# Optimization experiments

Measured on AMD Instinct MI355X. Metric: run time of the kernel, lower is better.

## Reference

```python
import jax, jax.numpy as jnp
import numpy as np

D = 1024   # rnn_size
H = 64     # pooling MLP hidden
B, C = 16, 1024


def setup_inputs() -> dict:
    key = jax.random.key(0)
    ks = jax.random.split(key, 12)
    s = 1.0 / np.sqrt(D)
    inp = {
        "encoder_outputs": jax.random.normal(ks[0], (B, C, D), jnp.float32),
        # Linear weights stored as [in, out] (y = x @ W + b), same math as torch Linear
        "Wf": jax.random.uniform(ks[1], (D, D), jnp.float32, -s, s),
        "bf": jax.random.uniform(ks[2], (D,), jnp.float32, -s, s),
        "Wg": jax.random.uniform(ks[3], (D, D), jnp.float32, -s, s),
        "bg": jax.random.uniform(ks[4], (D,), jnp.float32, -s, s),
        "Wx": jax.random.uniform(ks[5], (D, D), jnp.float32, -s, s),
        "bx": jax.random.uniform(ks[6], (D,), jnp.float32, -s, s),
        "W1": jax.random.uniform(ks[7], (D, H), jnp.float32, -s, s),
        "b1": jax.random.uniform(ks[8], (H,), jnp.float32, -s, s),
        "W2": jax.random.uniform(ks[9], (H, 1), jnp.float32, -1.0 / np.sqrt(H), 1.0 / np.sqrt(H)),
        "b2": jax.random.uniform(ks[10], (1,), jnp.float32, -1.0 / np.sqrt(H), 1.0 / np.sqrt(H)),
        # gamma is nn.Parameter(zeros(1)); use a nonzero value for a nontrivial baseline
        "gamma": jax.random.normal(ks[11], (1,), jnp.float32) * 0.1,
    }
    return inp


def reference(encoder_outputs, Wf, bf, Wg, bg, Wx, bx, W1, b1, W2, b2, gamma):
    x = encoder_outputs                                  # [B, C, D]
    q = jax.nn.relu(x @ Wf + bf)                         # proj_query [B, C, D]
    k = jax.nn.relu(x @ Wg + bg)                         # proj_key   [B, C, D]
    v = jax.nn.relu(x @ Wx + bx)                         # proj_value [B, C, D]
    energy = jnp.einsum('bid,bjd->bij', q, k)            # [B, C, C]
    attn = jax.nn.softmax(energy, axis=1)                # softmax over dim=1 (non-standard axis)
    # out = attention^T @ v : out[b,j,d] = sum_i attn[b,i,j] * v[b,i,d]
    out = jnp.einsum('bij,bid->bjd', attn, v)            # [B, C, D]
    out = gamma * out + x                                # gamma-residual
    # MLP attention pooling over C
    e2 = jax.nn.relu(x @ W1 + b1) @ W2 + b2              # [B, C, 1]
    w = jax.nn.softmax(e2[..., 0], axis=1)               # [B, C]
    return jnp.sum(out * w[..., None], axis=1)           # [B, D]
```

## Files before the change

### kernel.cpp

```cpp
#include <hip/hip_runtime.h>

#define B_ 16
#define C_ 1024
#define D_ 1024
#define H_ 64
#define M_ (B_*C_)

typedef __attribute__((ext_vector_type(8))) short bf16x8;
typedef __attribute__((ext_vector_type(8))) unsigned short ushortx8;
typedef __attribute__((ext_vector_type(4))) float f32x4;

__device__ __forceinline__ float wave_max(float v){
  #pragma unroll
  for (int o = 32; o > 0; o >>= 1) v = fmaxf(v, __shfl_xor(v, o));
  return v;
}
__device__ __forceinline__ float wave_sum(float v){
  #pragma unroll
  for (int o = 32; o > 0; o >>= 1) v += __shfl_xor(v, o);
  return v;
}

__device__ __forceinline__ ushort f2bf(float f){
  union { float f; unsigned u; } a; a.f = f;
  unsigned r = a.u + 0x7fff + ((a.u >> 16) & 1);
  return (ushort)(r >> 16);
}
__device__ __forceinline__ float bf2f(ushort h){
  union { unsigned u; float f; } a; a.u = ((unsigned)h) << 16; return a.f;
}

__device__ __forceinline__ void lds_cp16(const ushort* g, ushort* l){
  __builtin_amdgcn_global_load_lds(
      (const __attribute__((address_space(1))) void*)g,
      (__attribute__((address_space(3))) void*)l, 16, 0, 0);
}

__global__ __launch_bounds__(256) void prep_kernel(
    const float* __restrict__ x, const float* __restrict__ Wf,
    const float* __restrict__ Wg, const float* __restrict__ Wx,
    const float* __restrict__ W1,
    ushort* __restrict__ x_bf, ushort* __restrict__ wt,
    ushort* __restrict__ w1t)
{
  __shared__ float tile[32][33];
  const int blk = blockIdx.x;
  const int t = threadIdx.x;
  if (blk < 16384) {
    const int i = blk*256 + t;
    float4 v = ((const float4*)x)[i];
    ushort4 o;
    o.x = f2bf(v.x); o.y = f2bf(v.y); o.z = f2bf(v.z); o.w = f2bf(v.w);
    ((ushort4*)x_bf)[i] = o;
  } else if (blk < 16384 + 3072) {
    const int bb = blk - 16384;
    const int z = bb >> 10, rem = bb & 1023;
    const int n0 = (rem & 31)*32, k0 = (rem >> 5)*32;
    const float* W = (z == 0) ? Wf : (z == 1) ? Wg : Wx;
    ushort* Out = wt + (size_t)z*D_*D_;
    const int tx = t & 31, ty = t >> 5;
    #pragma unroll
    for (int i = 0; i < 32; i += 8)
      tile[ty+i][tx] = W[(size_t)(k0+ty+i)*D_ + n0+tx];
    __syncthreads();
    #pragma unroll
    for (int i = 0; i < 32; i += 8)
      Out[(size_t)(n0+ty+i)*D_ + k0+tx] = f2bf(tile[tx][ty+i]);
  } else {
    const int bb = blk - 16384 - 3072;
    const int n0 = (bb & 1)*32, k0 = (bb >> 1)*32;
    const int tx = t & 31, ty = t >> 5;
    #pragma unroll
    for (int i = 0; i < 32; i += 8)
      tile[ty+i][tx] = W1[(size_t)(k0+ty+i)*H_ + n0+tx];
    __syncthreads();
    #pragma unroll
    for (int i = 0; i < 32; i += 8)
      w1t[(size_t)(n0+ty+i)*D_ + k0+tx] = f2bf(tile[tx][ty+i]);
  }
}

__global__ __launch_bounds__(256, 3) void proj_kernel(
    const ushort* __restrict__ A, const ushort* __restrict__ Wt,
    const float* __restrict__ bf, const float* __restrict__ bg,
    const float* __restrict__ bx,
    ushort* __restrict__ q, ushort* __restrict__ k, ushort* __restrict__ v)
{
  __shared__ ushort As[128*64];
  __shared__ ushort Bs[128*64];
  const int t = threadIdx.x;
  const int wid = t >> 6, lane = t & 63;
  const int m0 = blockIdx.y * 128, n0 = blockIdx.x * 128;
  const int seg = n0 >> 10;
  const int nloc0 = n0 - (seg << 10);

  const int srow = t >> 3;
  const int sch = ((t & 7) ^ (srow & 7)) * 8;
  const ushort* gaBase = A  + (size_t)(m0 + srow)*1024 + sch;
  const ushort* gbBase = Wt + (size_t)(n0 + srow)*1024 + sch;

  const int quad = lane >> 4, l16 = lane & 15;
  const int wm = wid >> 1, wn = wid & 1;
  const int cx0 = ((0*4 + quad) ^ (l16 & 7)) * 8;
  const int cx1 = ((1*4 + quad) ^ (l16 & 7)) * 8;
  const int arow0 = (wm*64 + l16)*64;
  const int brow0 = (wn*64 + l16)*64;

  f32x4 acc[4][4] = {};

  for (int k0 = 0; k0 < 1024; k0 += 64) {
    #pragma unroll
    for (int i = 0; i < 4; ++i) {
      lds_cp16(gaBase + (size_t)(i*32)*1024, As + (8*wid + 32*i)*64);
      lds_cp16(gbBase + (size_t)(i*32)*1024, Bs + (8*wid + 32*i)*64);
    }
    gaBase += 64; gbBase += 64;
    __syncthreads();
    #pragma unroll
    for (int h = 0; h < 2; ++h) {
      const int cx = h ? cx1 : cx0;
      bf16x8 af[4], bfr[4];
      #pragma unroll
      for (int i = 0; i < 4; ++i) {
        af[i]  = *(const bf16x8*)&As[arow0 + i*1024 + cx];
        bfr[i] = *(const bf16x8*)&Bs[brow0 + i*1024 + cx];
      }
      #pragma unroll
      for (int mt = 0; mt < 4; ++mt)
        #pragma unroll
        for (int nt = 0; nt < 4; ++nt)
          acc[mt][nt] = __builtin_amdgcn_mfma_f32_16x16x32_bf16(
              af[mt], bfr[nt], acc[mt][nt], 0, 0, 0);
    }
    __syncthreads();
  }

  const float* bp = (seg == 0) ? bf : (seg == 1) ? bg : bx;
  ushort* op      = (seg == 0) ? q  : (seg == 1) ? k  : v;
  const int gm_base = m0 + wm*64 + quad*4;
  const int gn_base = nloc0 + wn*64 + l16;
  float bv[4];
  #pragma unroll
  for (int nt = 0; nt < 4; ++nt) bv[nt] = bp[gn_base + nt*16];
  #pragma unroll
  for (int mt = 0; mt < 4; ++mt)
    #pragma unroll
    for (int rr = 0; rr < 4; ++rr) {
      const size_t rowoff = (size_t)(gm_base + mt*16 + rr) * 1024;
      #pragma unroll
      for (int nt = 0; nt < 4; ++nt)
        op[rowoff + gn_base + nt*16] =
            f2bf(fmaxf(acc[mt][nt][rr] + bv[nt], 0.f));
    }
}

__global__ __launch_bounds__(256, 4) void energy_kernel(
    const ushort* __restrict__ Km, const ushort* __restrict__ Qm,
    ushort* __restrict__ E)
{
  __shared__ ushort As[64*64];
  __shared__ ushort Bs[128*64];
  const int t = threadIdx.x;
  const int wid = t >> 6, lane = t & 63;
  const int m0 = blockIdx.y * 64, n0 = blockIdx.x * 128;
  const int bz = blockIdx.z;
  const ushort* Ab = Km + (size_t)bz * C_ * D_;
  const ushort* Bb = Qm + (size_t)bz * C_ * D_;

  const int srow = t >> 3;
  const int sch = ((t & 7) ^ (srow & 7)) * 8;
  const ushort* gaBase = Ab + (size_t)(m0 + srow)*1024 + sch;
  const ushort* gbBase = Bb + (size_t)(n0 + srow)*1024 + sch;

  const int quad = lane >> 4, l16 = lane & 15;
  const int cx0 = ((0*4 + quad) ^ (l16 & 7)) * 8;
  const int cx1 = ((1*4 + quad) ^ (l16 & 7)) * 8;
  const int brow0 = (wid*32 + l16)*64;

  f32x4 acc[4][2] = {};

  for (int k0 = 0; k0 < 1024; k0 += 64) {
    #pragma unroll
    for (int i = 0; i < 2; ++i)
      lds_cp16(gaBase + (size_t)(i*32)*1024, As + (8*wid + 32*i)*64);
    #pragma unroll
    for (int i = 0; i < 4; ++i)
      lds_cp16(gbBase + (size_t)(i*32)*1024, Bs + (8*wid + 32*i)*64);
    gaBase += 64; gbBase += 64;
    __syncthreads();
    #pragma unroll
    for (int h = 0; h < 2; ++h) {
      const int cx = h ? cx1 : cx0;
      bf16x8 af[4], bfr[2];
      #pragma unroll
      for (int i = 0; i < 4; ++i)
        af[i] = *(const bf16x8*)&As[(i*16 + l16)*64 + cx];
      #pragma unroll
      for (int i = 0; i < 2; ++i)
        bfr[i] = *(const bf16x8*)&Bs[brow0 + i*16*64 + cx];
      #pragma unroll
      for (int mt = 0; mt < 4; ++mt)
        #pragma unroll
        for (int nt = 0; nt < 2; ++nt)
          acc[mt][nt] = __builtin_amdgcn_mfma_f32_16x16x32_bf16(
              af[mt], bfr[nt], acc[mt][nt], 0, 0, 0);
    }
    __syncthreads();
  }

  ushort* O = E + (size_t)bz * C_ * C_;
  const int gm_base = m0 + quad*4;
  const int gn_base = n0 + wid*32 + l16;
  #pragma unroll
  for (int mt = 0; mt < 4; ++mt)
    #pragma unroll
    for (int rr = 0; rr < 4; ++rr) {
      const size_t rowoff = (size_t)(gm_base + mt*16 + rr) * 1024;
      #pragma unroll
      for (int nt = 0; nt < 2; ++nt)
        O[rowoff + gn_base + nt*16] = f2bf(acc[mt][nt][rr]);
    }
}

__device__ __forceinline__ int fsw(int row){
  return (row & 3) ^ ((row >> 2) & 3);
}
__global__ __launch_bounds__(256) void pool_mfma_kernel(
    const ushort* __restrict__ A, const ushort* __restrict__ Bt,
    const float* __restrict__ b1, const float* __restrict__ W2,
    float* __restrict__ e2out)
{
  __shared__ ushort As[128*32];
  __shared__ ushort Bs[64*32];
  const int t = threadIdx.x;
  const int wid = t >> 6, lane = t & 63;
  const int m0 = blockIdx.x * 128;

  const int r = t >> 2;
  const int kc = ((t & 3) ^ fsw(r)) * 8;
  const ushort* ga0 = A + (size_t)(m0 + r)*1024 + kc;
  const ushort* ga1 = ga0 + (size_t)64*1024;
  const ushort* gb0 = Bt + (size_t)r*1024 + kc;
  ushort* lA = As + wid*512;
  ushort* lB = Bs + wid*512;

  const int quad = lane >> 4, l16 = lane & 15;
  const int fr = fsw(l16);
  const int am0 = (wid*32 + l16)*32 + ((quad ^ fr)*8);
  const int bn0 = l16*32 + ((quad ^ fr)*8);

  f32x4 acc[2][4] = {};

  for (int k0 = 0; k0 < 1024; k0 += 32) {
    lds_cp16(ga0, lA); lds_cp16(ga1, lA + 2048);
    lds_cp16(gb0, lB);
    ga0 += 32; ga1 += 32; gb0 += 32;
    __syncthreads();
    bf16x8 af[2], bfr[4];
    #pragma unroll
    for (int i = 0; i < 2; ++i) af[i] = *(const bf16x8*)&As[am0 + i*512];
    #pragma unroll
    for (int i = 0; i < 4; ++i) bfr[i] = *(const bf16x8*)&Bs[bn0 + i*512];
    #pragma unroll
    for (int mt = 0; mt < 2; ++mt)
      #pragma unroll
      for (int nt = 0; nt < 4; ++nt)
        acc[mt][nt] = __builtin_amdgcn_mfma_f32_16x16x32_bf16(
            af[mt], bfr[nt], acc[mt][nt], 0, 0, 0);
    __syncthreads();
  }

  float b1v[4], w2v[4];
  #pragma unroll
  for (int nt = 0; nt < 4; ++nt) {
    b1v[nt] = b1[nt*16 + l16];
    w2v[nt] = W2[nt*16 + l16];
  }
  #pragma unroll
  for (int mt = 0; mt < 2; ++mt)
    #pragma unroll
    for (int rr = 0; rr < 4; ++rr) {
      float h = 0.f;
      #pragma unroll
      for (int nt = 0; nt < 4; ++nt)
        h += fmaxf(acc[mt][nt][rr] + b1v[nt], 0.f) * w2v[nt];
      #pragma unroll
      for (int o = 1; o < 16; o <<= 1) h += __shfl_xor(h, o);
      if (l16 == 0)
        e2out[m0 + wid*32 + mt*16 + quad*4 + rr] = h;
    }
}

__global__ __launch_bounds__(256) void fused_sm_kernel(
    const ushort* __restrict__ E, const float* __restrict__ w,
    float* __restrict__ u_part)
{
  __shared__ float ul[4][1024];
  const int b = blockIdx.y;
  const int strip = blockIdx.x;
  const int t = threadIdx.x, wv = t >> 6, lane = t & 63;
  const ushort* Eb = E + (size_t)b*C_*C_;
  const float* wb = w + (size_t)b*C_;
  float acc[2][8] = {};
  #pragma unroll
  for (int rj = 0; rj < 4; ++rj) {
    const int j = strip*16 + wv*4 + rj;
    const ushort* row = Eb + (size_t)j*C_;
    float vv[2][8];
    float m = -1e30f;
    #pragma unroll
    for (int c = 0; c < 2; ++c) {
      ushortx8 h = *(const ushortx8*)&row[c*512 + lane*8];
      #pragma unroll
      for (int kk = 0; kk < 8; ++kk) {
        vv[c][kk] = bf2f(h[kk]);
        m = fmaxf(m, vv[c][kk]);
      }
    }
    m = wave_max(m);
    float e[2][8];
    float s = 0.f;
    #pragma unroll
    for (int c = 0; c < 2; ++c)
      #pragma unroll
      for (int kk = 0; kk < 8; ++kk) {
        e[c][kk] = expf(vv[c][kk] - m);
        s += e[c][kk];
      }
    s = wave_sum(s);
    const float sc = wb[j] / s;
    #pragma unroll
    for (int c = 0; c < 2; ++c)
      #pragma unroll
      for (int kk = 0; kk < 8; ++kk) acc[c][kk] += sc * e[c][kk];
  }
  #pragma unroll
  for (int c = 0; c < 2; ++c)
    #pragma unroll
    for (int k4 = 0; k4 < 2; ++k4) {
      float4 o;
      o.x = acc[c][k4*4+0]; o.y = acc[c][k4*4+1];
      o.z = acc[c][k4*4+2]; o.w = acc[c][k4*4+3];
      *(float4*)&ul[wv][c*512 + lane*8 + k4*4] = o;
    }
  __syncthreads();
  float4 r0 = *(float4*)&ul[0][t*4];
  float4 r1 = *(float4*)&ul[1][t*4];
  float4 r2 = *(float4*)&ul[2][t*4];
  float4 r3 = *(float4*)&ul[3][t*4];
  float4 o;
  o.x = r0.x+r1.x+r2.x+r3.x; o.y = r0.y+r1.y+r2.y+r3.y;
  o.z = r0.z+r1.z+r2.z+r3.z; o.w = r0.w+r1.w+r2.w+r3.w;
  *(float4*)&u_part[((size_t)strip*B_ + b)*C_ + t*4] = o;
}

__global__ __launch_bounds__(256) void softmax_w_kernel(
    const float* __restrict__ e2in, float* __restrict__ w)
{
  __shared__ float redm[4];
  __shared__ float reds[4];
  const int b = blockIdx.x, t = threadIdx.x;
  const int lane = t & 63, wid = t >> 6;
  const float* row = e2in + (size_t)b*C_;
  float4 v = *(const float4*)&row[t*4];
  float m = fmaxf(fmaxf(v.x, v.y), fmaxf(v.z, v.w));
  m = wave_max(m);
  if (lane == 0) redm[wid] = m;
  __syncthreads();
  m = fmaxf(fmaxf(redm[0], redm[1]), fmaxf(redm[2], redm[3]));
  float e0 = expf(v.x - m), e1 = expf(v.y - m);
  float e2 = expf(v.z - m), e3 = expf(v.w - m);
  float s = e0 + e1 + e2 + e3;
  s = wave_sum(s);
  if (lane == 0) reds[wid] = s;
  __syncthreads();
  s = reds[0] + reds[1] + reds[2] + reds[3];
  const float inv = 1.0f / s;
  float4 o; o.x = e0*inv; o.y = e1*inv; o.z = e2*inv; o.w = e3*inv;
  *(float4*)&w[(size_t)b*C_ + t*4] = o;
}

__global__ __launch_bounds__(256) void final_part_kernel(
    const ushort* __restrict__ X, const ushort* __restrict__ V,
    const float* __restrict__ u_part, const float* __restrict__ w,
    const float* __restrict__ gamma, float* __restrict__ fpart)
{
  const int b = blockIdx.x, s = blockIdx.y;
  const int t = threadIdx.x;
  __shared__ float red[16][17];
  __shared__ float us[16];
  {
    const int ii = t & 15, g = t >> 4;
    float p = 0.f;
    #pragma unroll
    for (int q2 = 0; q2 < 4; ++q2) {
      const int sp = g*4 + q2;
      p += u_part[((size_t)sp*B_ + b)*C_ + s*16 + ii];
    }
    red[ii][g] = p;
  }
  __syncthreads();
  if (t < 16) {
    float s2 = 0.f;
    #pragma unroll
    for (int g = 0; g < 16; ++g) s2 += red[t][g];
    us[t] = s2;
  }
  __syncthreads();

  const int d0 = t * 4;
  const ushort* xb = X + (size_t)b*C_*D_;
  const ushort* vb = V + (size_t)b*C_*D_;
  const float* wb = w + (size_t)b*C_;
  float4 av = {0,0,0,0}, ax = {0,0,0,0};
  #pragma unroll
  for (int ii = 0; ii < 16; ++ii) {
    const int i = s*16 + ii;
    const float ui = us[ii], wi = wb[i];
    ushort4 vv = *(const ushort4*)&vb[(size_t)i*D_ + d0];
    ushort4 xv = *(const ushort4*)&xb[(size_t)i*D_ + d0];
    av.x += ui*bf2f(vv.x); av.y += ui*bf2f(vv.y);
    av.z += ui*bf2f(vv.z); av.w += ui*bf2f(vv.w);
    ax.x += wi*bf2f(xv.x); ax.y += wi*bf2f(xv.y);
    ax.z += wi*bf2f(xv.z); ax.w += wi*bf2f(xv.w);
  }
  const float g = gamma[0];
  float4 o;
  o.x = g*av.x + ax.x; o.y = g*av.y + ax.y;
  o.z = g*av.z + ax.z; o.w = g*av.w + ax.w;
  *(float4*)&fpart[((size_t)s*B_ + b)*D_ + d0] = o;
}

__global__ __launch_bounds__(256) void final_combine_kernel(
    const float* __restrict__ fpart, float* __restrict__ out)
{
  const int idx = blockIdx.x*256 + threadIdx.x;
  float s = 0.f;
  #pragma unroll 8
  for (int sp = 0; sp < 64; ++sp) s += fpart[(size_t)sp*B_*D_ + idx];
  out[idx] = s;
}

extern "C" void kernel_launch(void* const* d_in, const int* in_sizes, int n_in,
                              void* d_out, int out_size, void* d_ws, size_t ws_size,
                              hipStream_t stream) {
  (void)in_sizes; (void)n_in; (void)out_size; (void)ws_size;
  const float* x  = (const float*)d_in[0];
  const float* Wf = (const float*)d_in[1];
  const float* bf = (const float*)d_in[2];
  const float* Wg = (const float*)d_in[3];
  const float* bg = (const float*)d_in[4];
  const float* Wx = (const float*)d_in[5];
  const float* bx = (const float*)d_in[6];
  const float* W1 = (const float*)d_in[7];
  const float* b1 = (const float*)d_in[8];
  const float* W2 = (const float*)d_in[9];
  const float* gamma = (const float*)d_in[11];
  float* out = (float*)d_out;

  ushort* x_bf = (ushort*)d_ws;
  ushort* wt   = x_bf + (size_t)M_*D_;
  ushort* w1t  = wt + (size_t)3*D_*D_;
  ushort* q_bf = w1t + (size_t)H_*D_;
  ushort* k_bf = q_bf + (size_t)M_*D_;
  ushort* v_bf = k_bf + (size_t)M_*D_;
  ushort* E    = v_bf + (size_t)M_*D_;
  float*  e2b  = (float*)(E + (size_t)B_*C_*C_);
  float*  wbuf = e2b + M_;
  float*  u_part = wbuf + M_;
  float*  fpart  = (float*)E;

  prep_kernel<<<dim3(16384+3072+64), 256, 0, stream>>>(
      x, Wf, Wg, Wx, W1, x_bf, wt, w1t);

  proj_kernel<<<dim3(24,128), 256, 0, stream>>>(x_bf, wt, bf, bg, bx,
                                                q_bf, k_bf, v_bf);

  pool_mfma_kernel<<<dim3(M_/128), 256, 0, stream>>>(x_bf, w1t, b1, W2, e2b);
  softmax_w_kernel<<<dim3(B_), 256, 0, stream>>>(e2b, wbuf);

  energy_kernel<<<dim3(8,16,B_), 256, 0, stream>>>(k_bf, q_bf, E);
  fused_sm_kernel<<<dim3(64,B_), 256, 0, stream>>>(E, wbuf, u_part);

  final_part_kernel<<<dim3(B_,64), 256, 0, stream>>>(x_bf, v_bf, u_part, wbuf,
                                                     gamma, fpart);
  final_combine_kernel<<<dim3(M_/256), 256, 0, stream>>>(fpart, out);
}
```

Measured before the change: 329.9 us.

## Rewrite projection GEMM with 256x256 tiles, 4-stage LDS pipeline and XCD swizzle

```diff
diff --git a/kernel.cpp b/kernel.cpp
--- a/kernel.cpp
+++ b/kernel.cpp
@@ -80,70 +80,113 @@
   }
 }
 
-__global__ __launch_bounds__(256, 3) void proj_kernel(
+__global__ __launch_bounds__(512, 2) void proj_kernel(
     const ushort* __restrict__ A, const ushort* __restrict__ Wt,
     const float* __restrict__ bf, const float* __restrict__ bg,
     const float* __restrict__ bx,
     ushort* __restrict__ q, ushort* __restrict__ k, ushort* __restrict__ v)
 {
-  __shared__ ushort As[128*64];
-  __shared__ ushort Bs[128*64];
+  __shared__ ushort As[4][8192];
+  __shared__ ushort Bs[4][8192];
   const int t = threadIdx.x;
-  const int wid = t >> 6, lane = t & 63;
-  const int m0 = blockIdx.y * 128, n0 = blockIdx.x * 128;
+  const int lane = t & 63;
+  const int wid  = t >> 6;
+  const int wm = wid >> 2;
+  const int wn = wid & 3;
+
+  const int wg = blockIdx.x;
+  const int sw = (wg & 7) * 96 + (wg >> 3);
+  const int mI = sw / 12, nI = sw - mI*12;
+  const int m0 = mI * 256, n0 = nI * 256;
   const int seg = n0 >> 10;
-  const int nloc0 = n0 - (seg << 10);
-
-  const int srow = t >> 3;
-  const int sch = ((t & 7) ^ (srow & 7)) * 8;
-  const ushort* gaBase = A  + (size_t)(m0 + srow)*1024 + sch;
-  const ushort* gbBase = Wt + (size_t)(n0 + srow)*1024 + sch;
+  const int nloc0 = n0 & 1023;
+
+  const int srow = t >> 2;
+  const int sfr  = (srow >> 1) & 3;
+  const int schunk = ((t & 3) ^ sfr) * 8;
+  const ushort* gA0 = A  + (size_t)(m0 + srow)*1024 + schunk;
+  const ushort* gA1 = gA0 + (size_t)128*1024;
+  const ushort* gB0 = Wt + (size_t)(n0 + srow)*1024 + schunk;
+  const ushort* gB1 = gB0 + (size_t)128*1024;
+  const int ldst = t * 8;
 
   const int quad = lane >> 4, l16 = lane & 15;
-  const int wm = wid >> 1, wn = wid & 1;
-  const int cx0 = ((0*4 + quad) ^ (l16 & 7)) * 8;
-  const int cx1 = ((1*4 + quad) ^ (l16 & 7)) * 8;
-  const int arow0 = (wm*64 + l16)*64;
-  const int brow0 = (wn*64 + l16)*64;
-
-  f32x4 acc[4][4] = {};
-
-  for (int k0 = 0; k0 < 1024; k0 += 64) {
-    #pragma unroll
-    for (int i = 0; i < 4; ++i) {
-      lds_cp16(gaBase + (size_t)(i*32)*1024, As + (8*wid + 32*i)*64);
-      lds_cp16(gbBase + (size_t)(i*32)*1024, Bs + (8*wid + 32*i)*64);
-    }
-    gaBase += 64; gbBase += 64;
-    __syncthreads();
-    #pragma unroll
-    for (int h = 0; h < 2; ++h) {
-      const int cx = h ? cx1 : cx0;
-      bf16x8 af[4], bfr[4];
-      #pragma unroll
-      for (int i = 0; i < 4; ++i) {
-        af[i]  = *(const bf16x8*)&As[arow0 + i*1024 + cx];
-        bfr[i] = *(const bf16x8*)&Bs[brow0 + i*1024 + cx];
-      }
-      #pragma unroll
-      for (int mt = 0; mt < 4; ++mt)
-        #pragma unroll
-        for (int nt = 0; nt < 4; ++nt)
-          acc[mt][nt] = __builtin_amdgcn_mfma_f32_16x16x32_bf16(
-              af[mt], bfr[nt], acc[mt][nt], 0, 0, 0);
-    }
-    __syncthreads();
+  const int fr4 = (l16 >> 1) & 3;
+  const int aoff = (wm*128 + l16)*32 + ((quad ^ fr4) * 8);
+  const int boff = (wn*64  + l16)*32 + ((quad ^ fr4) * 8);
+
+  f32x4 acc[8][4] = {};
+
+  #pragma unroll
+  for (int tt = 0; tt < 3; ++tt) {
+    const int ko = tt * 32;
+    lds_cp16(gA0 + ko, &As[tt][ldst]);
+    lds_cp16(gA1 + ko, &As[tt][4096 + ldst]);
+    lds_cp16(gB0 + ko, &Bs[tt][ldst]);
+    lds_cp16(gB1 + ko, &Bs[tt][4096 + ldst]);
+  }
+  asm volatile("s_waitcnt vmcnt(8)" ::: "memory");
+  __builtin_amdgcn_s_barrier();
+
+  for (int t0 = 0; t0 < 32; ++t0) {
+    const int cur = t0 & 3;
+    const ushort* Ab = As[cur];
+    const ushort* Bb = Bs[cur];
+    const int nxt = (t0 + 3) & 3;
+    const int ko  = (t0 + 3) * 32;
+
+    bf16x8 bfr[4], af[4];
+    #pragma unroll
+    for (int i = 0; i < 4; ++i) bfr[i] = *(const bf16x8*)&Bb[boff + i*512];
+    #pragma unroll
+    for (int i = 0; i < 4; ++i) af[i]  = *(const bf16x8*)&Ab[aoff + i*512];
+    if (t0 < 29) {
+      lds_cp16(gA0 + ko, &As[nxt][ldst]);
+      lds_cp16(gA1 + ko, &As[nxt][4096 + ldst]);
+    }
+    __builtin_amdgcn_s_barrier();
+    asm volatile("s_waitcnt lgkmcnt(0)" ::: "memory");
+    __builtin_amdgcn_s_setprio(1);
+    #pragma unroll
+    for (int mt = 0; mt < 4; ++mt)
+      #pragma unroll
+      for (int nt = 0; nt < 4; ++nt)
+        acc[mt][nt] = __builtin_amdgcn_mfma_f32_16x16x32_bf16(
+            af[mt], bfr[nt], acc[mt][nt], 0, 0, 0);
+    __builtin_amdgcn_s_setprio(0);
+    __builtin_amdgcn_s_barrier();
+
+    #pragma unroll
+    for (int i = 0; i < 4; ++i) af[i] = *(const bf16x8*)&Ab[aoff + 2048 + i*512];
+    if (t0 < 29) {
+      lds_cp16(gB0 + ko, &Bs[nxt][ldst]);
+      lds_cp16(gB1 + ko, &Bs[nxt][4096 + ldst]);
+    }
+    __builtin_amdgcn_s_barrier();
+    asm volatile("s_waitcnt lgkmcnt(0)" ::: "memory");
+    __builtin_amdgcn_s_setprio(1);
+    #pragma unroll
+    for (int mt = 0; mt < 4; ++mt)
+      #pragma unroll
+      for (int nt = 0; nt < 4; ++nt)
+        acc[4+mt][nt] = __builtin_amdgcn_mfma_f32_16x16x32_bf16(
+            af[mt], bfr[nt], acc[4+mt][nt], 0, 0, 0);
+    __builtin_amdgcn_s_setprio(0);
+    if (t0 < 29)       asm volatile("s_waitcnt vmcnt(8)" ::: "memory");
+    else if (t0 == 29) asm volatile("s_waitcnt vmcnt(4)" ::: "memory");
+    else if (t0 == 30) asm volatile("s_waitcnt vmcnt(0)" ::: "memory");
+    __builtin_amdgcn_s_barrier();
   }
 
   const float* bp = (seg == 0) ? bf : (seg == 1) ? bg : bx;
   ushort* op      = (seg == 0) ? q  : (seg == 1) ? k  : v;
-  const int gm_base = m0 + wm*64 + quad*4;
+  const int gm_base = m0 + wm*128 + quad*4;
   const int gn_base = nloc0 + wn*64 + l16;
   float bv[4];
   #pragma unroll
   for (int nt = 0; nt < 4; ++nt) bv[nt] = bp[gn_base + nt*16];
   #pragma unroll
-  for (int mt = 0; mt < 4; ++mt)
+  for (int mt = 0; mt < 8; ++mt)
     #pragma unroll
     for (int rr = 0; rr < 4; ++rr) {
       const size_t rowoff = (size_t)(gm_base + mt*16 + rr) * 1024;
@@ -473,8 +516,8 @@
   prep_kernel<<<dim3(16384+3072+64), 256, 0, stream>>>(
       x, Wf, Wg, Wx, W1, x_bf, wt, w1t);
 
-  proj_kernel<<<dim3(24,128), 256, 0, stream>>>(x_bf, wt, bf, bg, bx,
-                                                q_bf, k_bf, v_bf);
+  proj_kernel<<<dim3(768), 512, 0, stream>>>(x_bf, wt, bf, bg, bx,
+                                             q_bf, k_bf, v_bf);
 
   pool_mfma_kernel<<<dim3(M_/128), 256, 0, stream>>>(x_bf, w1t, b1, W2, e2b);
   softmax_w_kernel<<<dim3(B_), 256, 0, stream>>>(e2b, wbuf);
```

Result: no change. 331.9 us (+0.6%).

## Rewrite projection GEMM as 256x256 double-buffered pipelined tile kernel

Applied to the files above, without the earlier changes.

```diff
diff --git a/kernel.cpp b/kernel.cpp
--- a/kernel.cpp
+++ b/kernel.cpp
@@ -80,79 +80,130 @@
   }
 }
 
-__global__ __launch_bounds__(256, 3) void proj_kernel(
+
+#define PJ_BAR()  __builtin_amdgcn_s_barrier()
+#define PJ_LG0()  asm volatile("s_waitcnt lgkmcnt(0)" ::: "memory")
+#define PJ_VM(N)  asm volatile("s_waitcnt vmcnt(" #N ")" ::: "memory")
+#define PJ_LA(S,H) do { _Pragma("unroll") for (int mt_ = 0; mt_ < 4; ++mt_) { \
+    af[mt_][0] = *(const bf16x8*)&As[((S)*2+(H))*8192 + aof0 + mt_*512];      \
+    af[mt_][1] = *(const bf16x8*)&As[((S)*2+(H))*8192 + aof1 + mt_*512]; } } while(0)
+#define PJ_LB(DST,S,H) do { _Pragma("unroll") for (int nt_ = 0; nt_ < 2; ++nt_) { \
+    DST[nt_][0] = *(const bf16x8*)&Bs[((S)*2+(H))*8192 + bof0 + nt_*512];         \
+    DST[nt_][1] = *(const bf16x8*)&Bs[((S)*2+(H))*8192 + bof1 + nt_*512]; } } while(0)
+#define PJ_SA(S,H,KO) do {                                              \
+    lds_cp16(gA[H][0] + (KO), &As[((S)*2+(H))*8192 + ldst]);            \
+    lds_cp16(gA[H][1] + (KO), &As[((S)*2+(H))*8192 + 4096 + ldst]); } while(0)
+#define PJ_SB(S,H,KO) do {                                              \
+    lds_cp16(gB[H][0] + (KO), &Bs[((S)*2+(H))*8192 + ldst]);            \
+    lds_cp16(gB[H][1] + (KO), &Bs[((S)*2+(H))*8192 + 4096 + ldst]); } while(0)
+#define PJ_MM(MH,NH,BFR) do {                                           \
+    __builtin_amdgcn_s_setprio(1);                                      \
+    _Pragma("unroll") for (int mt_ = 0; mt_ < 4; ++mt_)                 \
+    _Pragma("unroll") for (int nt_ = 0; nt_ < 2; ++nt_) {               \
+      acc[(MH)*4+mt_][(NH)*2+nt_] = __builtin_amdgcn_mfma_f32_16x16x32_bf16( \
+          af[mt_][0], BFR[nt_][0], acc[(MH)*4+mt_][(NH)*2+nt_], 0, 0, 0);    \
+      acc[(MH)*4+mt_][(NH)*2+nt_] = __builtin_amdgcn_mfma_f32_16x16x32_bf16( \
+          af[mt_][1], BFR[nt_][1], acc[(MH)*4+mt_][(NH)*2+nt_], 0, 0, 0); }  \
+    __builtin_amdgcn_s_setprio(0); } while(0)
+
+__global__ __launch_bounds__(512, 2) void proj_kernel(
     const ushort* __restrict__ A, const ushort* __restrict__ Wt,
     const float* __restrict__ bf, const float* __restrict__ bg,
     const float* __restrict__ bx,
     ushort* __restrict__ q, ushort* __restrict__ k, ushort* __restrict__ v)
 {
-  __shared__ ushort As[128*64];
-  __shared__ ushort Bs[128*64];
+  __shared__ ushort As[2*2*8192];
+  __shared__ ushort Bs[2*2*8192];
   const int t = threadIdx.x;
-  const int wid = t >> 6, lane = t & 63;
-  const int m0 = blockIdx.y * 128, n0 = blockIdx.x * 128;
+  const int lane = t & 63;
+  const int wid  = t >> 6;
+  const int wm = wid >> 2;
+  const int wn = wid & 3;
+
+  const int wg = blockIdx.x;
+  const int sw = (wg & 7) * 96 + (wg >> 3);
+  const int mI = sw / 12, nI = sw - mI*12;
+  const int m0 = mI * 256, n0 = nI * 256;
   const int seg = n0 >> 10;
-  const int nloc0 = n0 - (seg << 10);
-
-  const int srow = t >> 3;
-  const int sch = ((t & 7) ^ (srow & 7)) * 8;
-  const ushort* gaBase = A  + (size_t)(m0 + srow)*1024 + sch;
-  const ushort* gbBase = Wt + (size_t)(n0 + srow)*1024 + sch;
+  const int nloc0 = n0 & 1023;
+
+  const int srow = t >> 2;
+  const int ldst = t * 8;
+  const ushort* gA[2][2];
+  const ushort* gB[2][2];
+  #pragma unroll
+  for (int h = 0; h < 2; ++h)
+    #pragma unroll
+    for (int j = 0; j < 2; ++j) {
+      const int lgc = ((j*4 + (t & 3)) ^ (srow & 7)) * 8;
+      gA[h][j] = A  + (size_t)(m0 + h*128 + srow)*1024 + lgc;
+      gB[h][j] = Wt + (size_t)(n0 + h*128 + srow)*1024 + lgc;
+    }
 
   const int quad = lane >> 4, l16 = lane & 15;
-  const int wm = wid >> 1, wn = wid & 1;
-  const int cx0 = ((0*4 + quad) ^ (l16 & 7)) * 8;
-  const int cx1 = ((1*4 + quad) ^ (l16 & 7)) * 8;
-  const int arow0 = (wm*64 + l16)*64;
-  const int brow0 = (wn*64 + l16)*64;
-
-  f32x4 acc[4][4] = {};
-
-  for (int k0 = 0; k0 < 1024; k0 += 64) {
-    #pragma unroll
-    for (int i = 0; i < 4; ++i) {
-      lds_cp16(gaBase + (size_t)(i*32)*1024, As + (8*wid + 32*i)*64);
-      lds_cp16(gbBase + (size_t)(i*32)*1024, Bs + (8*wid + 32*i)*64);
-    }
-    gaBase += 64; gbBase += 64;
-    __syncthreads();
-    #pragma unroll
-    for (int h = 0; h < 2; ++h) {
-      const int cx = h ? cx1 : cx0;
-      bf16x8 af[4], bfr[4];
-      #pragma unroll
-      for (int i = 0; i < 4; ++i) {
-        af[i]  = *(const bf16x8*)&As[arow0 + i*1024 + cx];
-        bfr[i] = *(const bf16x8*)&Bs[brow0 + i*1024 + cx];
-      }
-      #pragma unroll
-      for (int mt = 0; mt < 4; ++mt)
-        #pragma unroll
-        for (int nt = 0; nt < 4; ++nt)
-          acc[mt][nt] = __builtin_amdgcn_mfma_f32_16x16x32_bf16(
-              af[mt], bfr[nt], acc[mt][nt], 0, 0, 0);
-    }
-    __syncthreads();
-  }
+  const int phk0 = (0*4 + quad) ^ (l16 & 7);
+  const int phk1 = (1*4 + quad) ^ (l16 & 7);
+  const int aof0 = (phk0 >> 2)*4096 + (wm*64 + l16)*32 + (phk0 & 3)*8;
+  const int aof1 = (phk1 >> 2)*4096 + (wm*64 + l16)*32 + (phk1 & 3)*8;
+  const int bof0 = (phk0 >> 2)*4096 + (wn*32 + l16)*32 + (phk0 & 3)*8;
+  const int bof1 = (phk1 >> 2)*4096 + (wn*32 + l16)*32 + (phk1 & 3)*8;
+
+  f32x4 acc[8][4] = {};
+  bf16x8 af[4][2], bA[2][2], bB[2][2];
+
+  PJ_SA(0,0,0); PJ_SB(0,0,0); PJ_SB(0,1,0); PJ_SA(0,1,0);
+  PJ_VM(4);
+  PJ_BAR();
+
+  for (int tt = 0; tt < 15; ++tt) {
+    const int cur = tt & 1, nxt = cur ^ 1;
+    const int ko = (tt + 1) * 64;
+    PJ_LA(cur,0); PJ_LB(bA,cur,0); PJ_SA(nxt,0,ko);
+    PJ_BAR(); PJ_LG0(); PJ_MM(0,0,bA); PJ_VM(4); PJ_BAR();
+    PJ_LB(bB,cur,1); PJ_SB(nxt,0,ko);
+    PJ_BAR(); PJ_LG0(); PJ_MM(0,1,bB); PJ_VM(4); PJ_BAR();
+    PJ_LA(cur,1); PJ_SB(nxt,1,ko);
+    PJ_BAR(); PJ_LG0(); PJ_MM(1,0,bA); PJ_BAR();
+    PJ_SA(nxt,1,ko);
+    PJ_BAR(); PJ_LG0(); PJ_MM(1,1,bB); PJ_VM(4); PJ_BAR();
+  }
+  PJ_LA(1,0); PJ_LB(bA,1,0);
+  PJ_BAR(); PJ_LG0(); PJ_MM(0,0,bA); PJ_VM(2); PJ_BAR();
+  PJ_LB(bB,1,1);
+  PJ_BAR(); PJ_LG0(); PJ_MM(0,1,bB); PJ_VM(0); PJ_BAR();
+  PJ_LA(1,1);
+  PJ_BAR(); PJ_LG0(); PJ_MM(1,0,bA); PJ_BAR();
+  PJ_BAR(); PJ_LG0(); PJ_MM(1,1,bB);
 
   const float* bp = (seg == 0) ? bf : (seg == 1) ? bg : bx;
   ushort* op      = (seg == 0) ? q  : (seg == 1) ? k  : v;
-  const int gm_base = m0 + wm*64 + quad*4;
-  const int gn_base = nloc0 + wn*64 + l16;
+  const int nbase = nloc0 + wn*32 + l16;
   float bv[4];
   #pragma unroll
-  for (int nt = 0; nt < 4; ++nt) bv[nt] = bp[gn_base + nt*16];
-  #pragma unroll
-  for (int mt = 0; mt < 4; ++mt)
+  for (int ni = 0; ni < 4; ++ni)
+    bv[ni] = bp[nbase + (ni>>1)*128 + (ni&1)*16];
+  #pragma unroll
+  for (int mi = 0; mi < 8; ++mi) {
+    const int grow0 = m0 + (mi>>2)*128 + wm*64 + (mi&3)*16 + quad*4;
     #pragma unroll
     for (int rr = 0; rr < 4; ++rr) {
-      const size_t rowoff = (size_t)(gm_base + mt*16 + rr) * 1024;
-      #pragma unroll
-      for (int nt = 0; nt < 4; ++nt)
-        op[rowoff + gn_base + nt*16] =
-            f2bf(fmaxf(acc[mt][nt][rr] + bv[nt], 0.f));
-    }
-}
+      const size_t rowoff = (size_t)(grow0 + rr) * 1024;
+      #pragma unroll
+      for (int ni = 0; ni < 4; ++ni)
+        op[rowoff + nbase + (ni>>1)*128 + (ni&1)*16] =
+            f2bf(fmaxf(acc[mi][ni][rr] + bv[ni], 0.f));
+    }
+  }
+}
+
+#undef PJ_BAR
+#undef PJ_LG0
+#undef PJ_VM
+#undef PJ_LA
+#undef PJ_LB
+#undef PJ_SA
+#undef PJ_SB
+#undef PJ_MM
 
 __global__ __launch_bounds__(256, 4) void energy_kernel(
     const ushort* __restrict__ Km, const ushort* __restrict__ Qm,
@@ -473,8 +524,8 @@
   prep_kernel<<<dim3(16384+3072+64), 256, 0, stream>>>(
       x, Wf, Wg, Wx, W1, x_bf, wt, w1t);
 
-  proj_kernel<<<dim3(24,128), 256, 0, stream>>>(x_bf, wt, bf, bg, bx,
-                                                q_bf, k_bf, v_bf);
+  proj_kernel<<<dim3(768), 512, 0, stream>>>(x_bf, wt, bf, bg, bx,
+                                             q_bf, k_bf, v_bf);
 
   pool_mfma_kernel<<<dim3(M_/128), 256, 0, stream>>>(x_bf, w1t, b1, W2, e2b);
   softmax_w_kernel<<<dim3(B_), 256, 0, stream>>>(e2b, wbuf);
```

After: 339.0 us. 2.7% more time.
